# Kernel optimization log

Hardware: AMD Instinct MI355X
Metric: run time of the kernel (lower is better)

Reference implementation:

```python
import jax, jax.numpy as jnp
import numpy as np

N = 100000
E = 1600000
F_IN = 500
HID = 8
HEADS = 8
C = 7
NEG_SLOPE = 0.2


def setup_inputs() -> dict:
    key = jax.random.key(0)
    ks = jax.random.split(key, 10)
    x = jax.random.normal(ks[0], (N, F_IN), dtype=jnp.float32)
    edge_index = jax.random.randint(ks[1], (2, E), 0, N, dtype=jnp.int64)
    # conv1 params: lin [heads*hid, F_in], att_src/att_dst [heads, hid], bias [heads*hid]
    s1 = 1.0 / np.sqrt(F_IN)
    W1 = jax.random.normal(ks[2], (HEADS * HID, F_IN), dtype=jnp.float32) * s1
    att_src1 = jax.random.normal(ks[3], (HEADS, HID), dtype=jnp.float32) * 0.1
    att_dst1 = jax.random.normal(ks[4], (HEADS, HID), dtype=jnp.float32) * 0.1
    b1 = jnp.zeros((HEADS * HID,), dtype=jnp.float32)
    # conv2 params: in = heads*hid, out = heads*C (concat=True)
    s2 = 1.0 / np.sqrt(HEADS * HID)
    W2 = jax.random.normal(ks[5], (HEADS * C, HEADS * HID), dtype=jnp.float32) * s2
    att_src2 = jax.random.normal(ks[6], (HEADS, C), dtype=jnp.float32) * 0.1
    att_dst2 = jax.random.normal(ks[7], (HEADS, C), dtype=jnp.float32) * 0.1
    b2 = jnp.zeros((HEADS * C,), dtype=jnp.float32)
    return {"x": x, "edge_index": edge_index, "W1": W1, "att_src1": att_src1,
            "att_dst1": att_dst1, "b1": b1, "W2": W2, "att_src2": att_src2,
            "att_dst2": att_dst2, "b2": b2}


def _gat_layer(h_in, src, dst, W, a_src, a_dst, b, heads, out_ch):
    n = h_in.shape[0]
    h = (h_in @ W.T).reshape(n, heads, out_ch)                 # [N,H,D]
    alpha_s = jnp.sum(h * a_src[None], axis=-1)                # [N,H]
    alpha_d = jnp.sum(h * a_dst[None], axis=-1)                # [N,H]
    e = jax.nn.leaky_relu(alpha_s[src] + alpha_d[dst], NEG_SLOPE)  # [E,H]
    # segment softmax over incoming edges of each dst node
    emax = jax.ops.segment_max(e, dst, num_segments=n)
    ee = jnp.exp(e - emax[dst])
    denom = jax.ops.segment_sum(ee, dst, num_segments=n)
    alpha = ee / denom[dst]                                    # [E,H]
    msg = h[src] * alpha[:, :, None]                           # [E,H,D]
    out = jax.ops.segment_sum(msg, dst, num_segments=n)        # [N,H,D]
    return out.reshape(n, heads * out_ch) + b


def reference(x, edge_index, W1, att_src1, att_dst1, b1, W2, att_src2, att_dst2, b2):
    n = x.shape[0]
    # PyG GATConv adds self-loops by default
    loop = jnp.arange(n, dtype=edge_index.dtype)
    src = jnp.concatenate([edge_index[0], loop])
    dst = jnp.concatenate([edge_index[1], loop])
    # dropout(p=0.6) is identity in eval mode
    h = _gat_layer(x, src, dst, W1, att_src1, att_dst1, b1, HEADS, HID)
    h = jax.nn.elu(h)
    out = _gat_layer(h, src, dst, W2, att_src2, att_dst2, b2, HEADS, C)
    return out  # [N, heads*num_classes]
```

## Files before the change

kernel.cpp:

```cpp
#include <hip/hip_runtime.h>

#define NEG_SLOPE 0.2f

typedef __bf16 bf16x8 __attribute__((ext_vector_type(8)));
typedef float f32x4 __attribute__((ext_vector_type(4)));

__device__ __forceinline__ float eluf(float x) { return x > 0.f ? x : __expf(x) - 1.f; }
__device__ __forceinline__ float lreluf(float x) { return x > 0.f ? x : NEG_SLOPE * x; }
__device__ __forceinline__ float bflo(unsigned u) { return __uint_as_float(u << 16); }
__device__ __forceinline__ float bfhi(unsigned u) { return __uint_as_float(u & 0xffff0000u); }

__device__ __forceinline__ void split8(const float4& p, const float4& q, bf16x8& hi, bf16x8& lo) {
  float v[8] = {p.x, p.y, p.z, p.w, q.x, q.y, q.z, q.w};
#pragma unroll
  for (int e = 0; e < 8; ++e) {
    __bf16 h = (__bf16)v[e];
    hi[e] = h;
    lo[e] = (__bf16)(v[e] - (float)h);
  }
}


__global__ __launch_bounds__(256) void k_convert(const int* __restrict__ raw,
                                                 int* __restrict__ out, int n) {
  int i = blockIdx.x * 256 + threadIdx.x;
  if (i >= n) return;
  int probe = 0;
#pragma unroll
  for (int t = 1; t < 64; t += 2) probe |= raw[t];
  bool is32 = probe != 0;
  out[i] = is32 ? raw[i] : raw[2 * i];
}

__global__ __launch_bounds__(256) void k_fill_shard(const int* __restrict__ ei, int* __restrict__ cnt,
                                                    int* __restrict__ csr, int E, int N, int CH) {
  const int shard = blockIdx.x & 7;
  const int chunk = blockIdx.x >> 3;
  const int i0 = chunk * CH;
  const int i1 = min(i0 + CH, E + N);
  for (int idx = i0 + (int)threadIdx.x; idx < i1; idx += 256) {
    int d = (idx < E) ? ei[E + idx] : idx - E;
    if (((d >> 13) & 7) != shard) continue;
    int s = (idx < E) ? ei[idx] : idx - E;
    int pos = atomicAdd(&cnt[d], 1);
    if (pos < 64) csr[(size_t)d * 64 + pos] = s;
  }
}


__global__ __launch_bounds__(256) void k_prep(const float* __restrict__ W1,
                                              __bf16* __restrict__ b1h, __bf16* __restrict__ b1l,
                                              const float* __restrict__ W2, const float* __restrict__ as2,
                                              const float* __restrict__ ad2,
                                              __bf16* __restrict__ b2h, __bf16* __restrict__ b2l) {
  int idx = blockIdx.x * 256 + threadIdx.x;
  if (idx < 32768) {
    int e = idx & 7;
    int lane = (idx >> 3) & 63;
    int nf = (idx >> 9) & 3;
    int ks = idx >> 11;
    int k = ks * 32 + (lane >> 4) * 8 + e;
    int col = nf * 16 + (lane & 15);
    float w = (k < 500) ? W1[(size_t)col * 500 + k] : 0.f;
    __bf16 hh = (__bf16)w;
    b1h[idx] = hh;
    b1l[idx] = (__bf16)(w - (float)hh);
  }
  if (idx < 5120) {
    int e = idx & 7;
    int lane = (idx >> 3) & 63;
    int nf = (idx >> 9) % 5;
    int ks = idx / 2560;
    int k = ks * 32 + (lane >> 4) * 8 + e;
    int c16 = lane & 15;
    float w = 0.f;
    if (nf < 4) {
      int col = nf * 16 + c16;
      if (col < 56) w = W2[(size_t)col * 64 + k];
    } else {
      const float* a = (c16 < 8) ? as2 : ad2;
      int h = c16 & 7;
      float s = 0.f;
#pragma unroll
      for (int d = 0; d < 7; ++d) s = fmaf(a[h * 7 + d], W2[(size_t)(h * 7 + d) * 64 + k], s);
      w = s;
    }
    __bf16 hh = (__bf16)w;
    b2h[idx] = hh;
    b2l[idx] = (__bf16)(w - (float)hh);
  }
}

__global__ __launch_bounds__(256) void k_gemm1_lds(const float* __restrict__ X, const bf16x8* __restrict__ Bhi,
                                                   const bf16x8* __restrict__ Blo,
                                                   const float* __restrict__ at_s, const float* __restrict__ at_d,
                                                   __bf16* __restrict__ outb,
                                                   float* __restrict__ as_, float* __restrict__ ad_, int M) {
  __shared__ __align__(16) float xs[3][2048];
  __shared__ __align__(16) __bf16 bs[3][4096];
  const int lane = threadIdx.x & 63;
  const int wid = threadIdx.x >> 6;
  const int row0 = blockIdx.x * 64;
  const int kgrp = lane >> 4;
  const int rloc = lane & 15;
  const int myrow = wid * 16 + rloc;

  const int ub = myrow * 128 + kgrp * 32;
  const int sw1 = (ub ^ ((myrow & 7) << 4)) >> 2;
  const int sw2 = ((ub + 16) ^ ((myrow & 7) << 4)) >> 2;

  int st_r[2], st_kf[2];
#pragma unroll
  for (int j = 0; j < 2; ++j) {
    int s = (wid * 2 + j) * 1024 + lane * 16;
    int r = s >> 7;
    int kb = (s & 127) ^ ((r & 7) << 4);
    st_r[j] = min(row0 + r, M - 1);
    st_kf[j] = kb >> 2;
  }

  auto stage = [&](int buf, int ks) {
#pragma unroll
    for (int j = 0; j < 2; ++j) {
      const float* src = X + (size_t)st_r[j] * 500 + ks * 32 + st_kf[j];
      __builtin_amdgcn_global_load_lds(
          (const __attribute__((address_space(1))) void*)src,
          (__attribute__((address_space(3))) void*)&xs[buf][(wid * 2 + j) * 256], 16, 0, 0);
    }
    const bf16x8* sh = Bhi + (size_t)(ks * 4 + wid) * 64 + lane;
    const bf16x8* sl = Blo + (size_t)(ks * 4 + wid) * 64 + lane;
    __builtin_amdgcn_global_load_lds(
        (const __attribute__((address_space(1))) void*)sh,
        (__attribute__((address_space(3))) void*)&bs[buf][wid * 512], 16, 0, 0);
    __builtin_amdgcn_global_load_lds(
        (const __attribute__((address_space(1))) void*)sl,
        (__attribute__((address_space(3))) void*)&bs[buf][2048 + wid * 512], 16, 0, 0);
  };

  f32x4 acc[4];
#pragma unroll
  for (int nf = 0; nf < 4; ++nf) acc[nf] = (f32x4){0.f, 0.f, 0.f, 0.f};

  stage(0, 0);
  stage(1, 1);
  asm volatile("s_waitcnt vmcnt(4)" ::: "memory");
  __builtin_amdgcn_s_barrier();
  __builtin_amdgcn_sched_barrier(0);

  for (int ks = 0; ks < 15; ++ks) {
    if (ks < 13) stage((ks + 2) % 3, ks + 2);
    const int b = ks % 3;
    float4 p = *reinterpret_cast<const float4*>(&xs[b][sw1]);
    float4 q = *reinterpret_cast<const float4*>(&xs[b][sw2]);
    bf16x8 ah, al;
    split8(p, q, ah, al);
#pragma unroll
    for (int nf = 0; nf < 4; ++nf) {
      bf16x8 bh = *reinterpret_cast<const bf16x8*>(&bs[b][nf * 512 + lane * 8]);
      bf16x8 bl = *reinterpret_cast<const bf16x8*>(&bs[b][2048 + nf * 512 + lane * 8]);
      acc[nf] = __builtin_amdgcn_mfma_f32_16x16x32_bf16(ah, bh, acc[nf], 0, 0, 0);
      acc[nf] = __builtin_amdgcn_mfma_f32_16x16x32_bf16(al, bh, acc[nf], 0, 0, 0);
      acc[nf] = __builtin_amdgcn_mfma_f32_16x16x32_bf16(ah, bl, acc[nf], 0, 0, 0);
    }
    if (ks < 14) {
      if (ks < 13) asm volatile("s_waitcnt vmcnt(4)" ::: "memory");
      else         asm volatile("s_waitcnt vmcnt(0)" ::: "memory");
      __builtin_amdgcn_s_barrier();
      __builtin_amdgcn_sched_barrier(0);
    }
  }

  {
    const bool rowok = row0 + myrow < M;
    const float* xrow = X + (size_t)(row0 + myrow) * 500;
    float v[8];
#pragma unroll
    for (int e = 0; e < 8; ++e) {
      int k = 480 + kgrp * 8 + e;
      v[e] = (rowok && k < 500) ? xrow[k] : 0.f;
    }
    bf16x8 ah, al;
#pragma unroll
    for (int e = 0; e < 8; ++e) {
      __bf16 h = (__bf16)v[e];
      ah[e] = h;
      al[e] = (__bf16)(v[e] - (float)h);
    }
#pragma unroll
    for (int nf = 0; nf < 4; ++nf) {
      bf16x8 bh = Bhi[(15 * 4 + nf) * 64 + lane];
      bf16x8 bl = Blo[(15 * 4 + nf) * 64 + lane];
      acc[nf] = __builtin_amdgcn_mfma_f32_16x16x32_bf16(ah, bh, acc[nf], 0, 0, 0);
      acc[nf] = __builtin_amdgcn_mfma_f32_16x16x32_bf16(al, bh, acc[nf], 0, 0, 0);
      acc[nf] = __builtin_amdgcn_mfma_f32_16x16x32_bf16(ah, bl, acc[nf], 0, 0, 0);
    }
  }

  const int colw = lane & 15;
  const int hi8 = colw >> 3, dd = colw & 7;
  float aS[4], aD[4];
#pragma unroll
  for (int nf = 0; nf < 4; ++nf) {
    aS[nf] = at_s[(nf * 2 + hi8) * 8 + dd];
    aD[nf] = at_d[(nf * 2 + hi8) * 8 + dd];
  }
#pragma unroll
  for (int r = 0; r < 4; ++r) {
    int rowd = row0 + wid * 16 + kgrp * 4 + r;
    bool ok = rowd < M;
    float ps[4], pd[4];
#pragma unroll
    for (int nf = 0; nf < 4; ++nf) {
      ps[nf] = acc[nf][r] * aS[nf];
      pd[nf] = acc[nf][r] * aD[nf];
    }
#pragma unroll
    for (int off = 1; off < 8; off <<= 1) {
#pragma unroll
      for (int nf = 0; nf < 4; ++nf) {
        ps[nf] += __shfl_xor(ps[nf], off);
        pd[nf] += __shfl_xor(pd[nf], off);
      }
    }
    if (ok) {
#pragma unroll
      for (int nf = 0; nf < 4; ++nf)
        outb[(size_t)rowd * 64 + nf * 16 + colw] = (__bf16)acc[nf][r];
      if (dd == 0) {
#pragma unroll
        for (int nf = 0; nf < 4; ++nf) {
          int head = nf * 2 + hi8;
          as_[(size_t)rowd * 8 + head] = ps[nf];
          ad_[(size_t)rowd * 8 + head] = pd[nf];
        }
      }
    }
  }
}

__global__ __launch_bounds__(256) void k_gemm2_mfma(const __bf16* __restrict__ Xh, const __bf16* __restrict__ Xl,
                                                    const bf16x8* __restrict__ B2h, const bf16x8* __restrict__ B2l,
                                                    __bf16* __restrict__ outb,
                                                    float* __restrict__ as_, float* __restrict__ ad_, int M) {
  __shared__ __align__(16) __bf16 xh[4096], xl[4096];
  const int lane = threadIdx.x & 63;
  const int wid = threadIdx.x >> 6;
  const int row0 = blockIdx.x * 64;
  const int kgrp = lane >> 4;
  const int rloc = lane & 15;
  const int myrow = wid * 16 + rloc;

#pragma unroll
  for (int j = 0; j < 4; ++j) {
    int chunk = wid * 4 + j;
    bool lo = chunk >= 8;
    int s = (chunk & 7) * 1024 + lane * 16;
    int r = s >> 7;
    int kb = (s & 127) ^ ((r & 7) << 4);
    int rg = min(row0 + r, M - 1);
    const __bf16* src = (lo ? Xl : Xh) + (size_t)rg * 64 + (kb >> 1);
    __bf16* dstbase = (lo ? xl : xh) + (chunk & 7) * 512;
    __builtin_amdgcn_global_load_lds(
        (const __attribute__((address_space(1))) void*)src,
        (__attribute__((address_space(3))) void*)dstbase, 16, 0, 0);
  }
  __syncthreads();

  f32x4 acc[5];
#pragma unroll
  for (int nf = 0; nf < 5; ++nf) acc[nf] = (f32x4){0.f, 0.f, 0.f, 0.f};

#pragma unroll
  for (int ks = 0; ks < 2; ++ks) {
    int ub = myrow * 128 + ks * 64 + kgrp * 16;
    int sw = (ub ^ ((myrow & 7) << 4)) >> 1;
    bf16x8 ah = *reinterpret_cast<const bf16x8*>(&xh[sw]);
    bf16x8 al = *reinterpret_cast<const bf16x8*>(&xl[sw]);
#pragma unroll
    for (int nf = 0; nf < 5; ++nf) {
      bf16x8 bh = B2h[(ks * 5 + nf) * 64 + lane];
      bf16x8 bl = B2l[(ks * 5 + nf) * 64 + lane];
      acc[nf] = __builtin_amdgcn_mfma_f32_16x16x32_bf16(ah, bh, acc[nf], 0, 0, 0);
      acc[nf] = __builtin_amdgcn_mfma_f32_16x16x32_bf16(al, bh, acc[nf], 0, 0, 0);
      acc[nf] = __builtin_amdgcn_mfma_f32_16x16x32_bf16(ah, bl, acc[nf], 0, 0, 0);
    }
  }

  const int colw = lane & 15;
#pragma unroll
  for (int r = 0; r < 4; ++r) {
    int rowd = row0 + wid * 16 + (lane >> 4) * 4 + r;
    if (rowd >= M) continue;
#pragma unroll
    for (int nf = 0; nf < 4; ++nf) {
      int col = nf * 16 + colw;
      if (col < 56) {
        int hh = col / 7, cc = col - hh * 7;
        outb[(size_t)rowd * 64 + hh * 8 + cc] = (__bf16)acc[nf][r];
      } else {
        outb[(size_t)rowd * 64 + (col - 56) * 8 + 7] = (__bf16)0.f;
      }
    }
    float av = acc[4][r];
    if (colw < 8) as_[(size_t)rowd * 8 + colw] = av;
    else          ad_[(size_t)rowd * 8 + (colw - 8)] = av;
  }
}

__global__ __launch_bounds__(256) void k_agg1v(const unsigned short* __restrict__ hb,
                                               const float* __restrict__ as_,
                                               const float* __restrict__ ad_,
                                               const int* __restrict__ cnt,
                                               const int* __restrict__ csr,
                                               const float* __restrict__ b1,
                                               __bf16* __restrict__ oh, __bf16* __restrict__ ol, int N) {
  const int lane = threadIdx.x & 63;
  const int n = blockIdx.x * 4 + (threadIdx.x >> 6);
  if (n >= N) return;
  const int r0 = n << 6;
  const int r1 = r0 + min(cnt[n], 64);
  const int head = lane & 7;
  const int slot = lane >> 3;
  const float ad_h = ad_[(size_t)n * 8 + head];

  float den0 = 0.f, den1 = 0.f;
  f32x4 A0 = {0.f, 0.f, 0.f, 0.f}, B0 = {0.f, 0.f, 0.f, 0.f};
  f32x4 A1 = {0.f, 0.f, 0.f, 0.f}, B1 = {0.f, 0.f, 0.f, 0.f};
  int j = r0 + slot;
  for (; j + 8 < r1; j += 16) {
    int s0 = csr[j], s1 = csr[j + 8];
    float p0 = __expf(lreluf(as_[(size_t)s0 * 8 + head] + ad_h));
    float p1 = __expf(lreluf(as_[(size_t)s1 * 8 + head] + ad_h));
    uint4 w0 = *reinterpret_cast<const uint4*>(hb + (size_t)s0 * 64 + head * 8);
    uint4 w1 = *reinterpret_cast<const uint4*>(hb + (size_t)s1 * 64 + head * 8);
    den0 += p0;
    den1 += p1;
    A0[0] = fmaf(p0, bflo(w0.x), A0[0]); A0[1] = fmaf(p0, bfhi(w0.x), A0[1]);
    A0[2] = fmaf(p0, bflo(w0.y), A0[2]); A0[3] = fmaf(p0, bfhi(w0.y), A0[3]);
    B0[0] = fmaf(p0, bflo(w0.z), B0[0]); B0[1] = fmaf(p0, bfhi(w0.z), B0[1]);
    B0[2] = fmaf(p0, bflo(w0.w), B0[2]); B0[3] = fmaf(p0, bfhi(w0.w), B0[3]);
    A1[0] = fmaf(p1, bflo(w1.x), A1[0]); A1[1] = fmaf(p1, bfhi(w1.x), A1[1]);
    A1[2] = fmaf(p1, bflo(w1.y), A1[2]); A1[3] = fmaf(p1, bfhi(w1.y), A1[3]);
    B1[0] = fmaf(p1, bflo(w1.z), B1[0]); B1[1] = fmaf(p1, bfhi(w1.z), B1[1]);
    B1[2] = fmaf(p1, bflo(w1.w), B1[2]); B1[3] = fmaf(p1, bfhi(w1.w), B1[3]);
  }
  if (j < r1) {
    int s0 = csr[j];
    float p0 = __expf(lreluf(as_[(size_t)s0 * 8 + head] + ad_h));
    uint4 w0 = *reinterpret_cast<const uint4*>(hb + (size_t)s0 * 64 + head * 8);
    den0 += p0;
    A0[0] = fmaf(p0, bflo(w0.x), A0[0]); A0[1] = fmaf(p0, bfhi(w0.x), A0[1]);
    A0[2] = fmaf(p0, bflo(w0.y), A0[2]); A0[3] = fmaf(p0, bfhi(w0.y), A0[3]);
    B0[0] = fmaf(p0, bflo(w0.z), B0[0]); B0[1] = fmaf(p0, bfhi(w0.z), B0[1]);
    B0[2] = fmaf(p0, bflo(w0.w), B0[2]); B0[3] = fmaf(p0, bfhi(w0.w), B0[3]);
  }
  float den = den0 + den1;
#pragma unroll
  for (int k = 0; k < 4; ++k) {
    A0[k] += A1[k];
    B0[k] += B1[k];
  }
#pragma unroll
  for (int off = 8; off < 64; off <<= 1) {
    den += __shfl_xor(den, off);
#pragma unroll
    for (int k = 0; k < 4; ++k) {
      A0[k] += __shfl_xor(A0[k], off);
      B0[k] += __shfl_xor(B0[k], off);
    }
  }
  if (lane < 8) {
    float inv_den = 1.f / den;
    float o[8];
#pragma unroll
    for (int k = 0; k < 4; ++k) {
      o[k] = eluf(A0[k] * inv_den + b1[lane * 8 + k]);
      o[4 + k] = eluf(B0[k] * inv_den + b1[lane * 8 + 4 + k]);
    }
    bf16x8 vh, vl;
#pragma unroll
    for (int k = 0; k < 8; ++k) {
      __bf16 h = (__bf16)o[k];
      vh[k] = h;
      vl[k] = (__bf16)(o[k] - (float)h);
    }
    *reinterpret_cast<bf16x8*>(oh + (size_t)n * 64 + lane * 8) = vh;
    *reinterpret_cast<bf16x8*>(ol + (size_t)n * 64 + lane * 8) = vl;
  }
}

__global__ __launch_bounds__(256) void k_agg2v(const unsigned short* __restrict__ hb,
                                               const float* __restrict__ as_,
                                               const float* __restrict__ ad_,
                                               const int* __restrict__ cnt,
                                               const int* __restrict__ csr,
                                               const float* __restrict__ bias,
                                               float* __restrict__ out, int N) {
  const int lane = threadIdx.x & 63;
  const int n = blockIdx.x * 4 + (threadIdx.x >> 6);
  if (n >= N) return;
  const int r0 = n << 6;
  const int r1 = r0 + min(cnt[n], 64);
  const int head = lane & 7;
  const int slot = lane >> 3;
  const float ad_h = ad_[(size_t)n * 8 + head];

  float den0 = 0.f, den1 = 0.f;
  f32x4 A0 = {0.f, 0.f, 0.f, 0.f}, B0 = {0.f, 0.f, 0.f, 0.f};
  f32x4 A1 = {0.f, 0.f, 0.f, 0.f}, B1 = {0.f, 0.f, 0.f, 0.f};
  int j = r0 + slot;
  for (; j + 8 < r1; j += 16) {
    int s0 = csr[j], s1 = csr[j + 8];
    float p0 = __expf(lreluf(as_[(size_t)s0 * 8 + head] + ad_h));
    float p1 = __expf(lreluf(as_[(size_t)s1 * 8 + head] + ad_h));
    uint4 w0 = *reinterpret_cast<const uint4*>(hb + (size_t)s0 * 64 + head * 8);
    uint4 w1 = *reinterpret_cast<const uint4*>(hb + (size_t)s1 * 64 + head * 8);
    den0 += p0;
    den1 += p1;
    A0[0] = fmaf(p0, bflo(w0.x), A0[0]); A0[1] = fmaf(p0, bfhi(w0.x), A0[1]);
    A0[2] = fmaf(p0, bflo(w0.y), A0[2]); A0[3] = fmaf(p0, bfhi(w0.y), A0[3]);
    B0[0] = fmaf(p0, bflo(w0.z), B0[0]); B0[1] = fmaf(p0, bfhi(w0.z), B0[1]);
    B0[2] = fmaf(p0, bflo(w0.w), B0[2]);
    A1[0] = fmaf(p1, bflo(w1.x), A1[0]); A1[1] = fmaf(p1, bfhi(w1.x), A1[1]);
    A1[2] = fmaf(p1, bflo(w1.y), A1[2]); A1[3] = fmaf(p1, bfhi(w1.y), A1[3]);
    B1[0] = fmaf(p1, bflo(w1.z), B1[0]); B1[1] = fmaf(p1, bfhi(w1.z), B1[1]);
    B1[2] = fmaf(p1, bflo(w1.w), B1[2]);
  }
  if (j < r1) {
    int s0 = csr[j];
    float p0 = __expf(lreluf(as_[(size_t)s0 * 8 + head] + ad_h));
    uint4 w0 = *reinterpret_cast<const uint4*>(hb + (size_t)s0 * 64 + head * 8);
    den0 += p0;
    A0[0] = fmaf(p0, bflo(w0.x), A0[0]); A0[1] = fmaf(p0, bfhi(w0.x), A0[1]);
    A0[2] = fmaf(p0, bflo(w0.y), A0[2]); A0[3] = fmaf(p0, bfhi(w0.y), A0[3]);
    B0[0] = fmaf(p0, bflo(w0.z), B0[0]); B0[1] = fmaf(p0, bfhi(w0.z), B0[1]);
    B0[2] = fmaf(p0, bflo(w0.w), B0[2]);
  }
  float den = den0 + den1;
#pragma unroll
  for (int k = 0; k < 4; ++k) {
    A0[k] += A1[k];
    B0[k] += B1[k];
  }
#pragma unroll
  for (int off = 8; off < 64; off <<= 1) {
    den += __shfl_xor(den, off);
#pragma unroll
    for (int k = 0; k < 4; ++k) {
      A0[k] += __shfl_xor(A0[k], off);
      B0[k] += __shfl_xor(B0[k], off);
    }
  }
  if (lane < 8) {
    float inv_den = 1.f / den;
    float* orow = out + (size_t)n * 56 + head * 7;
    const float* brow = bias + head * 7;
    orow[0] = A0[0] * inv_den + brow[0];
    orow[1] = A0[1] * inv_den + brow[1];
    orow[2] = A0[2] * inv_den + brow[2];
    orow[3] = A0[3] * inv_den + brow[3];
    orow[4] = B0[0] * inv_den + brow[4];
    orow[5] = B0[1] * inv_den + brow[5];
    orow[6] = B0[2] * inv_den + brow[6];
  }
}


extern "C" void kernel_launch(void* const* d_in, const int* in_sizes, int n_in,
                              void* d_out, int out_size, void* d_ws, size_t ws_size,
                              hipStream_t stream) {
  const float* x    = (const float*)d_in[0];
  const int*   ei   = (const int*)d_in[1];
  const float* W1   = (const float*)d_in[2];
  const float* at_s1 = (const float*)d_in[3];
  const float* at_d1 = (const float*)d_in[4];
  const float* b1   = (const float*)d_in[5];
  const float* W2   = (const float*)d_in[6];
  const float* at_s2 = (const float*)d_in[7];
  const float* at_d2 = (const float*)d_in[8];
  const float* b2   = (const float*)d_in[9];
  float* out = (float*)d_out;

  const int N = in_sizes[0] / 500;
  const int E = in_sizes[1] / 2;

  char* w = (char*)d_ws;
  auto alloc = [&](size_t bytes) -> void* {
    void* p = (void*)w;
    w += (bytes + 255) & ~(size_t)255;
    return p;
  };
  int*   cnt    = (int*)alloc((size_t)N * 4);
  int*   ei_c   = (int*)alloc((size_t)2 * E * 4);
  int*   csr    = (int*)alloc((size_t)N * 64 * 4);
  float* asb    = (float*)alloc((size_t)N * 8 * 4);
  float* adb    = (float*)alloc((size_t)N * 8 * 4);
  __bf16* B1h   = (__bf16*)alloc((size_t)32768 * 2);
  __bf16* B1l   = (__bf16*)alloc((size_t)32768 * 2);
  __bf16* B2h   = (__bf16*)alloc((size_t)5120 * 2);
  __bf16* B2l   = (__bf16*)alloc((size_t)5120 * 2);
  __bf16* h1b   = (__bf16*)alloc((size_t)N * 64 * 2);
  __bf16* o1h   = (__bf16*)alloc((size_t)N * 64 * 2);
  __bf16* o1l   = (__bf16*)alloc((size_t)N * 64 * 2);
  __bf16* h2b   = (__bf16*)alloc((size_t)N * 64 * 2);

  auto cdiv = [](int a, int b) { return (a + b - 1) / b; };

  hipMemsetAsync(cnt, 0, (size_t)N * 4, stream);
  k_convert<<<cdiv(2 * E, 256), 256, 0, stream>>>(ei, ei_c, 2 * E);
  {
    const int G = 768;
    k_fill_shard<<<8 * G, 256, 0, stream>>>(ei_c, cnt, csr, E, N, cdiv(E + N, G));
  }

  k_prep<<<128, 256, 0, stream>>>(W1, B1h, B1l, W2, at_s2, at_d2, B2h, B2l);

  k_gemm1_lds<<<cdiv(N, 64), 256, 0, stream>>>(x, (const bf16x8*)B1h, (const bf16x8*)B1l,
                                               at_s1, at_d1, h1b, asb, adb, N);
  k_agg1v<<<cdiv(N, 4), 256, 0, stream>>>((const unsigned short*)h1b, asb, adb, cnt, csr, b1, o1h, o1l, N);

  k_gemm2_mfma<<<cdiv(N, 64), 256, 0, stream>>>(o1h, o1l, (const bf16x8*)B2h, (const bf16x8*)B2l, h2b, asb, adb, N);
  k_agg2v<<<cdiv(N, 4), 256, 0, stream>>>((const unsigned short*)h2b, asb, adb, cnt, csr, b2, out, N);
}
```

Before: 283.4 us.

## Fuse edge-index conversion into CSR fill and pack source logits into feature rows

```diff
diff --git a/kernel.cpp b/kernel.cpp
--- a/kernel.cpp
+++ b/kernel.cpp
@@ -9,6 +9,7 @@
 __device__ __forceinline__ float lreluf(float x) { return x > 0.f ? x : NEG_SLOPE * x; }
 __device__ __forceinline__ float bflo(unsigned u) { return __uint_as_float(u << 16); }
 __device__ __forceinline__ float bfhi(unsigned u) { return __uint_as_float(u & 0xffff0000u); }
+__device__ __forceinline__ float bfval(unsigned short u) { return __uint_as_float((unsigned)u << 16); }
 
 __device__ __forceinline__ void split8(const float4& p, const float4& q, bf16x8& hi, bf16x8& lo) {
   float v[8] = {p.x, p.y, p.z, p.w, q.x, q.y, q.z, q.w};
@@ -21,27 +22,20 @@
 }
 
 
-__global__ __launch_bounds__(256) void k_convert(const int* __restrict__ raw,
-                                                 int* __restrict__ out, int n) {
-  int i = blockIdx.x * 256 + threadIdx.x;
-  if (i >= n) return;
+__global__ __launch_bounds__(256) void k_fill_shard(const int* __restrict__ raw, int* __restrict__ cnt,
+                                                    int* __restrict__ csr, int E, int N, int CH) {
   int probe = 0;
 #pragma unroll
   for (int t = 1; t < 64; t += 2) probe |= raw[t];
-  bool is32 = probe != 0;
-  out[i] = is32 ? raw[i] : raw[2 * i];
-}
-
-__global__ __launch_bounds__(256) void k_fill_shard(const int* __restrict__ ei, int* __restrict__ cnt,
-                                                    int* __restrict__ csr, int E, int N, int CH) {
+  const bool is32 = probe != 0;
   const int shard = blockIdx.x & 7;
   const int chunk = blockIdx.x >> 3;
   const int i0 = chunk * CH;
   const int i1 = min(i0 + CH, E + N);
   for (int idx = i0 + (int)threadIdx.x; idx < i1; idx += 256) {
-    int d = (idx < E) ? ei[E + idx] : idx - E;
+    int d = (idx < E) ? (is32 ? raw[E + idx] : raw[2 * (E + idx)]) : idx - E;
     if (((d >> 13) & 7) != shard) continue;
-    int s = (idx < E) ? ei[idx] : idx - E;
+    int s = (idx < E) ? (is32 ? raw[idx] : raw[2 * idx]) : idx - E;
     int pos = atomicAdd(&cnt[d], 1);
     if (pos < 64) csr[(size_t)d * 64 + pos] = s;
   }
@@ -95,7 +89,7 @@
                                                    const bf16x8* __restrict__ Blo,
                                                    const float* __restrict__ at_s, const float* __restrict__ at_d,
                                                    __bf16* __restrict__ outb,
-                                                   float* __restrict__ as_, float* __restrict__ ad_, int M) {
+                                                   __bf16* __restrict__ as1b, float* __restrict__ ad_, int M) {
   __shared__ __align__(16) float xs[3][2048];
   __shared__ __align__(16) __bf16 bs[3][4096];
   const int lane = threadIdx.x & 63;
@@ -230,7 +224,7 @@
 #pragma unroll
         for (int nf = 0; nf < 4; ++nf) {
           int head = nf * 2 + hi8;
-          as_[(size_t)rowd * 8 + head] = ps[nf];
+          as1b[(size_t)rowd * 8 + head] = (__bf16)ps[nf];
           ad_[(size_t)rowd * 8 + head] = pd[nf];
         }
       }
@@ -241,7 +235,7 @@
 __global__ __launch_bounds__(256) void k_gemm2_mfma(const __bf16* __restrict__ Xh, const __bf16* __restrict__ Xl,
                                                     const bf16x8* __restrict__ B2h, const bf16x8* __restrict__ B2l,
                                                     __bf16* __restrict__ outb,
-                                                    float* __restrict__ as_, float* __restrict__ ad_, int M) {
+                                                    float* __restrict__ ad_, int M) {
   __shared__ __align__(16) __bf16 xh[4096], xl[4096];
   const int lane = threadIdx.x & 63;
   const int wid = threadIdx.x >> 6;
@@ -289,6 +283,8 @@
   const int colw = lane & 15;
 #pragma unroll
   for (int r = 0; r < 4; ++r) {
+    float av = acc[4][r];
+    float av_x = __shfl_xor(av, 8);
     int rowd = row0 + wid * 16 + (lane >> 4) * 4 + r;
     if (rowd >= M) continue;
 #pragma unroll
@@ -298,17 +294,15 @@
         int hh = col / 7, cc = col - hh * 7;
         outb[(size_t)rowd * 64 + hh * 8 + cc] = (__bf16)acc[nf][r];
       } else {
-        outb[(size_t)rowd * 64 + (col - 56) * 8 + 7] = (__bf16)0.f;
+        outb[(size_t)rowd * 64 + (col - 56) * 8 + 7] = (__bf16)av_x;
       }
     }
-    float av = acc[4][r];
-    if (colw < 8) as_[(size_t)rowd * 8 + colw] = av;
-    else          ad_[(size_t)rowd * 8 + (colw - 8)] = av;
+    if (colw >= 8) ad_[(size_t)rowd * 8 + (colw - 8)] = av;
   }
 }
 
 __global__ __launch_bounds__(256) void k_agg1v(const unsigned short* __restrict__ hb,
-                                               const float* __restrict__ as_,
+                                               const unsigned short* __restrict__ as1b,
                                                const float* __restrict__ ad_,
                                                const int* __restrict__ cnt,
                                                const int* __restrict__ csr,
@@ -329,8 +323,8 @@
   int j = r0 + slot;
   for (; j + 8 < r1; j += 16) {
     int s0 = csr[j], s1 = csr[j + 8];
-    float p0 = __expf(lreluf(as_[(size_t)s0 * 8 + head] + ad_h));
-    float p1 = __expf(lreluf(as_[(size_t)s1 * 8 + head] + ad_h));
+    float p0 = __expf(lreluf(bfval(as1b[(size_t)s0 * 8 + head]) + ad_h));
+    float p1 = __expf(lreluf(bfval(as1b[(size_t)s1 * 8 + head]) + ad_h));
     uint4 w0 = *reinterpret_cast<const uint4*>(hb + (size_t)s0 * 64 + head * 8);
     uint4 w1 = *reinterpret_cast<const uint4*>(hb + (size_t)s1 * 64 + head * 8);
     den0 += p0;
@@ -346,7 +340,7 @@
   }
   if (j < r1) {
     int s0 = csr[j];
-    float p0 = __expf(lreluf(as_[(size_t)s0 * 8 + head] + ad_h));
+    float p0 = __expf(lreluf(bfval(as1b[(size_t)s0 * 8 + head]) + ad_h));
     uint4 w0 = *reinterpret_cast<const uint4*>(hb + (size_t)s0 * 64 + head * 8);
     den0 += p0;
     A0[0] = fmaf(p0, bflo(w0.x), A0[0]); A0[1] = fmaf(p0, bfhi(w0.x), A0[1]);
@@ -390,7 +384,6 @@
 }
 
 __global__ __launch_bounds__(256) void k_agg2v(const unsigned short* __restrict__ hb,
-                                               const float* __restrict__ as_,
                                                const float* __restrict__ ad_,
                                                const int* __restrict__ cnt,
                                                const int* __restrict__ csr,
@@ -411,10 +404,10 @@
   int j = r0 + slot;
   for (; j + 8 < r1; j += 16) {
     int s0 = csr[j], s1 = csr[j + 8];
-    float p0 = __expf(lreluf(as_[(size_t)s0 * 8 + head] + ad_h));
-    float p1 = __expf(lreluf(as_[(size_t)s1 * 8 + head] + ad_h));
     uint4 w0 = *reinterpret_cast<const uint4*>(hb + (size_t)s0 * 64 + head * 8);
     uint4 w1 = *reinterpret_cast<const uint4*>(hb + (size_t)s1 * 64 + head * 8);
+    float p0 = __expf(lreluf(bfhi(w0.w) + ad_h));
+    float p1 = __expf(lreluf(bfhi(w1.w) + ad_h));
     den0 += p0;
     den1 += p1;
     A0[0] = fmaf(p0, bflo(w0.x), A0[0]); A0[1] = fmaf(p0, bfhi(w0.x), A0[1]);
@@ -428,8 +421,8 @@
   }
   if (j < r1) {
     int s0 = csr[j];
-    float p0 = __expf(lreluf(as_[(size_t)s0 * 8 + head] + ad_h));
     uint4 w0 = *reinterpret_cast<const uint4*>(hb + (size_t)s0 * 64 + head * 8);
+    float p0 = __expf(lreluf(bfhi(w0.w) + ad_h));
     den0 += p0;
     A0[0] = fmaf(p0, bflo(w0.x), A0[0]); A0[1] = fmaf(p0, bfhi(w0.x), A0[1]);
     A0[2] = fmaf(p0, bflo(w0.y), A0[2]); A0[3] = fmaf(p0, bfhi(w0.y), A0[3]);
@@ -491,10 +484,9 @@
     return p;
   };
   int*   cnt    = (int*)alloc((size_t)N * 4);
-  int*   ei_c   = (int*)alloc((size_t)2 * E * 4);
   int*   csr    = (int*)alloc((size_t)N * 64 * 4);
-  float* asb    = (float*)alloc((size_t)N * 8 * 4);
   float* adb    = (float*)alloc((size_t)N * 8 * 4);
+  __bf16* as1b  = (__bf16*)alloc((size_t)N * 8 * 2);
   __bf16* B1h   = (__bf16*)alloc((size_t)32768 * 2);
   __bf16* B1l   = (__bf16*)alloc((size_t)32768 * 2);
   __bf16* B2h   = (__bf16*)alloc((size_t)5120 * 2);
@@ -507,18 +499,18 @@
   auto cdiv = [](int a, int b) { return (a + b - 1) / b; };
 
   hipMemsetAsync(cnt, 0, (size_t)N * 4, stream);
-  k_convert<<<cdiv(2 * E, 256), 256, 0, stream>>>(ei, ei_c, 2 * E);
   {
     const int G = 768;
-    k_fill_shard<<<8 * G, 256, 0, stream>>>(ei_c, cnt, csr, E, N, cdiv(E + N, G));
+    k_fill_shard<<<8 * G, 256, 0, stream>>>(ei, cnt, csr, E, N, cdiv(E + N, G));
   }
 
   k_prep<<<128, 256, 0, stream>>>(W1, B1h, B1l, W2, at_s2, at_d2, B2h, B2l);
 
   k_gemm1_lds<<<cdiv(N, 64), 256, 0, stream>>>(x, (const bf16x8*)B1h, (const bf16x8*)B1l,
-                                               at_s1, at_d1, h1b, asb, adb, N);
-  k_agg1v<<<cdiv(N, 4), 256, 0, stream>>>((const unsigned short*)h1b, asb, adb, cnt, csr, b1, o1h, o1l, N);
-
-  k_gemm2_mfma<<<cdiv(N, 64), 256, 0, stream>>>(o1h, o1l, (const bf16x8*)B2h, (const bf16x8*)B2l, h2b, asb, adb, N);
-  k_agg2v<<<cdiv(N, 4), 256, 0, stream>>>((const unsigned short*)h2b, asb, adb, cnt, csr, b2, out, N);
-}
+                                               at_s1, at_d1, h1b, as1b, adb, N);
+  k_agg1v<<<cdiv(N, 4), 256, 0, stream>>>((const unsigned short*)h1b, (const unsigned short*)as1b,
+                                          adb, cnt, csr, b1, o1h, o1l, N);
+
+  k_gemm2_mfma<<<cdiv(N, 64), 256, 0, stream>>>(o1h, o1l, (const bf16x8*)B2h, (const bf16x8*)B2l, h2b, adb, N);
+  k_agg2v<<<cdiv(N, 4), 256, 0, stream>>>((const unsigned short*)h2b, adb, cnt, csr, b2, out, N);
+}
```

After: 260.8 us. -8.0%, faster.
